# Optimization experiments

Hardware: AMD Instinct MI355X
Metric: run time of the kernel (lower is better)

## Reference

```python
import jax, jax.numpy as jnp
import numpy as np

MARGIN = 0.3
HARD_FACTOR = 0.0
EPS = 1e-6


def setup_inputs() -> dict:
    key = jax.random.key(0)
    k1, k2 = jax.random.split(key)
    inputs = jax.random.normal(k1, (4096, 256), dtype=jnp.float32)
    targets = jax.random.randint(k2, (4096,), 0, 512, dtype=jnp.int64)
    return {"inputs": inputs, "targets": targets}


def reference(inputs, targets):
    n = inputs.shape[0]
    half = n // 2
    # L2-normalize features (matches normalize(): x / (||x|| + 1e-6))
    x = inputs / (jnp.linalg.norm(inputs, axis=-1, keepdims=True) + EPS)
    # pairwise euclidean distances, clamped at 1e-6 before sqrt
    sq = jnp.sum(x * x, axis=1)                      # (n,)
    dist = sq[:, None] + sq[None, :] - 2.0 * (x @ x.T)  # (n, n)
    dist = jnp.sqrt(jnp.clip(dist, EPS))
    # same-identity mask
    mask = targets[:, None] == targets[None, :]      # (n, n) bool
    # rows in the first half mine over columns [half:n], rows in the
    # second half mine over columns [0:half] -> gather the opposite half
    first = (jnp.arange(n) < half)[:, None]          # (n, 1)
    d_o = jnp.where(first, dist[:, half:], dist[:, :half])  # (n, half)
    m_o = jnp.where(first, mask[:, half:], mask[:, :half])  # (n, half) bool
    pos_any = jnp.any(m_o, axis=1)
    neg_any = jnp.any(~m_o, axis=1)
    dist_ap = jnp.where(pos_any,
                        jnp.max(jnp.where(m_o, d_o, -jnp.inf), axis=1),
                        0.0)
    dist_an = jnp.where(neg_any,
                        jnp.min(jnp.where(m_o, jnp.inf, d_o), axis=1),
                        1.0)
    dist_ap = dist_ap * (1.0 + HARD_FACTOR)
    dist_an = dist_an * (1.0 - HARD_FACTOR)
    # MarginRankingLoss(margin)(dist_an, dist_ap, y=1) =
    #   mean(relu(-(dist_an - dist_ap) + margin))
    loss = jnp.mean(jax.nn.relu(dist_ap - dist_an + MARGIN))
    return loss
```

## Files before the change

### kernel.cpp

```cpp
#include <hip/hip_runtime.h>
#include <math.h>

#define N 4096
#define D 256
#define HALF 2048
#define MARGIN 0.3f

#define BM 64
#define NTB (HALF/BM)
#define LDA 264

typedef __attribute__((ext_vector_type(8))) short bf16x8;
typedef __attribute__((ext_vector_type(4))) float f32x4;

__device__ __forceinline__ unsigned short bf16_rne(float x) {
    unsigned int u = __float_as_uint(x);
    return (unsigned short)((u + 0x7fffu + ((u >> 16) & 1u)) >> 16);
}

__global__ __launch_bounds__(256) void k_norm(const float* __restrict__ in,
                                              unsigned short* __restrict__ xnb,
                                              float* __restrict__ sq,
                                              float* __restrict__ acc_sum,
                                              int* __restrict__ acc_cnt) {
    const int wave = threadIdx.x >> 6, lane = threadIdx.x & 63;
    const int row = blockIdx.x * 4 + wave;
    float4 v = *(const float4*)&in[(size_t)row * D + lane * 4];
    float s = v.x * v.x + v.y * v.y + v.z * v.z + v.w * v.w;
#pragma unroll
    for (int o = 1; o < 64; o <<= 1) s += __shfl_xor(s, o, 64);
    float nrm = sqrtf(s);
    float inv = 1.0f / (nrm + 1e-6f);
    ushort4 h;
    h.x = bf16_rne(v.x * inv);
    h.y = bf16_rne(v.y * inv);
    h.z = bf16_rne(v.z * inv);
    h.w = bf16_rne(v.w * inv);
    *(ushort4*)&xnb[(size_t)row * D + lane * 4] = h;
    if (lane == 0) {
        float q = nrm * inv;
        sq[row] = q * q;
    }
    if (blockIdx.x == 0 && threadIdx.x == 0) {
        *acc_sum = 0.f;
        *acc_cnt = 0;
    }
}

__global__ __launch_bounds__(256) void k_tile(const unsigned short* __restrict__ xnb,
                                              const float* __restrict__ sq,
                                              const int* __restrict__ tg,
                                              float* __restrict__ rowap,
                                              float* __restrict__ rowan,
                                              float* __restrict__ colap,
                                              float* __restrict__ colan) {
    __shared__ unsigned short As[BM * LDA];
    __shared__ unsigned short Bs[BM * LDA];
    __shared__ int sra[BM], srn[BM], sca[BM], scn[BM];

    const int bi = blockIdx.y, bj = blockIdx.x;
    const int I0 = bi * BM;
    const int J0 = bj * BM;
    const int tid = threadIdx.x;
    const int wave = tid >> 6, lane = tid & 63;
    const int wm = wave >> 1, wn = wave & 1;
    const int lrow = lane & 15, lquad = lane >> 4;

    {
        const int chunk = tid & 31;
        const int rp = tid >> 5;
        const unsigned short* Agp = xnb + (size_t)I0 * D;
        const unsigned short* Bgp = xnb + (size_t)(HALF + J0) * D;
        uint4 av[8], bv[8];
#pragma unroll
        for (int i = 0; i < 8; ++i) {
            int r = i * 8 + rp;
            av[i] = *(const uint4*)&Agp[(size_t)r * D + chunk * 8];
            bv[i] = *(const uint4*)&Bgp[(size_t)r * D + chunk * 8];
        }
#pragma unroll
        for (int i = 0; i < 8; ++i) {
            int r = i * 8 + rp;
            *(uint4*)&As[r * LDA + chunk * 8] = av[i];
            *(uint4*)&Bs[r * LDA + chunk * 8] = bv[i];
        }
    }
    __syncthreads();

    f32x4 acc[2][2];
#pragma unroll
    for (int a = 0; a < 2; ++a)
#pragma unroll
        for (int b = 0; b < 2; ++b) acc[a][b] = (f32x4){0.f, 0.f, 0.f, 0.f};

#pragma unroll
    for (int k0 = 0; k0 < D; k0 += 32) {
        bf16x8 af[2], bfr[2];
#pragma unroll
        for (int mi = 0; mi < 2; ++mi)
            af[mi] = *(const bf16x8*)&As[(wm * 32 + mi * 16 + lrow) * LDA + k0 + lquad * 8];
#pragma unroll
        for (int nj = 0; nj < 2; ++nj)
            bfr[nj] = *(const bf16x8*)&Bs[(wn * 32 + nj * 16 + lrow) * LDA + k0 + lquad * 8];
#pragma unroll
        for (int mi = 0; mi < 2; ++mi)
#pragma unroll
            for (int nj = 0; nj < 2; ++nj)
                acc[mi][nj] = __builtin_amdgcn_mfma_f32_16x16x32_bf16(
                    af[mi], bfr[nj], acc[mi][nj], 0, 0, 0);
    }

    float sqi[2][4], sqj[2];
    int tgi[2][4], tgj[2];
#pragma unroll
    for (int mi = 0; mi < 2; ++mi)
#pragma unroll
        for (int r = 0; r < 4; ++r) {
            int lr = wm * 32 + mi * 16 + lquad * 4 + r;
            sqi[mi][r] = sq[I0 + lr];
            tgi[mi][r] = tg[I0 + lr];
        }
#pragma unroll
    for (int nj = 0; nj < 2; ++nj) {
        int lc = wn * 32 + nj * 16 + lrow;
        sqj[nj] = sq[HALF + J0 + lc];
        tgj[nj] = tg[HALF + J0 + lc];
    }

    const float INF = __int_as_float(0x7f800000);
    float rap[2][4], ran[2][4], capv[2], canv[2];
#pragma unroll
    for (int mi = 0; mi < 2; ++mi)
#pragma unroll
        for (int r = 0; r < 4; ++r) { rap[mi][r] = 0.f; ran[mi][r] = INF; }
#pragma unroll
    for (int nj = 0; nj < 2; ++nj) { capv[nj] = 0.f; canv[nj] = INF; }

#pragma unroll
    for (int mi = 0; mi < 2; ++mi)
#pragma unroll
        for (int nj = 0; nj < 2; ++nj)
#pragma unroll
            for (int r = 0; r < 4; ++r) {
                float d2 = sqi[mi][r] + sqj[nj] - 2.0f * acc[mi][nj][r];
                float d = sqrtf(fmaxf(d2, 1e-6f));
                if (tgi[mi][r] == tgj[nj]) {
                    rap[mi][r] = fmaxf(rap[mi][r], d);
                    capv[nj] = fmaxf(capv[nj], d);
                } else {
                    ran[mi][r] = fminf(ran[mi][r], d);
                    canv[nj] = fminf(canv[nj], d);
                }
            }

#pragma unroll
    for (int mi = 0; mi < 2; ++mi)
#pragma unroll
        for (int r = 0; r < 4; ++r)
#pragma unroll
            for (int o = 1; o < 16; o <<= 1) {
                rap[mi][r] = fmaxf(rap[mi][r], __shfl_xor(rap[mi][r], o, 64));
                ran[mi][r] = fminf(ran[mi][r], __shfl_xor(ran[mi][r], o, 64));
            }
#pragma unroll
    for (int nj = 0; nj < 2; ++nj)
#pragma unroll
        for (int o = 16; o < 64; o <<= 1) {
            capv[nj] = fmaxf(capv[nj], __shfl_xor(capv[nj], o, 64));
            canv[nj] = fminf(canv[nj], __shfl_xor(canv[nj], o, 64));
        }

    if (tid < BM) { sra[tid] = 0; srn[tid] = 0x7f800000;
                    sca[tid] = 0; scn[tid] = 0x7f800000; }
    __syncthreads();
    if (lrow == 0) {
#pragma unroll
        for (int mi = 0; mi < 2; ++mi)
#pragma unroll
            for (int r = 0; r < 4; ++r) {
                int lr = wm * 32 + mi * 16 + lquad * 4 + r;
                atomicMax(&sra[lr], __float_as_int(rap[mi][r]));
                atomicMin(&srn[lr], __float_as_int(ran[mi][r]));
            }
    }
    if (lquad == 0) {
#pragma unroll
        for (int nj = 0; nj < 2; ++nj) {
            int lc = wn * 32 + nj * 16 + lrow;
            atomicMax(&sca[lc], __float_as_int(capv[nj]));
            atomicMin(&scn[lc], __float_as_int(canv[nj]));
        }
    }
    __syncthreads();
    if (tid < BM) {
        rowap[bj * HALF + I0 + tid] = __int_as_float(sra[tid]);
        rowan[bj * HALF + I0 + tid] = __int_as_float(srn[tid]);
        colap[bi * HALF + J0 + tid] = __int_as_float(sca[tid]);
        colan[bi * HALF + J0 + tid] = __int_as_float(scn[tid]);
    }
}

__global__ __launch_bounds__(64) void k_reduce(const float* __restrict__ rowap,
                                               const float* __restrict__ rowan,
                                               const float* __restrict__ colap,
                                               const float* __restrict__ colan,
                                               float* __restrict__ acc_sum,
                                               int* __restrict__ acc_cnt,
                                               float* __restrict__ out) {
    const int lane = threadIdx.x;
    const int gid = blockIdx.x * 64 + lane;
    const float INF = __int_as_float(0x7f800000);
    float ap = 0.f, an = INF;
    if (gid < HALF) {
#pragma unroll
        for (int b = 0; b < NTB; ++b) {
            ap = fmaxf(ap, rowap[b * HALF + gid]);
            an = fminf(an, rowan[b * HALF + gid]);
        }
    } else {
        int j = gid - HALF;
#pragma unroll
        for (int b = 0; b < NTB; ++b) {
            ap = fmaxf(ap, colap[b * HALF + j]);
            an = fminf(an, colan[b * HALF + j]);
        }
    }
    if (an == INF) an = 1.0f;
    float v = ap - an + MARGIN;
    float s = (v > 0.f) ? v : 0.f;
#pragma unroll
    for (int o = 1; o < 64; o <<= 1) s += __shfl_xor(s, o, 64);
    if (lane == 0) {
        atomicAdd(acc_sum, s);
        __threadfence();
        int old = atomicAdd(acc_cnt, 1);
        if (old == 63) {
            float tot = atomicAdd(acc_sum, 0.0f);
            out[0] = tot / (float)N;
        }
    }
}

extern "C" void kernel_launch(void* const* d_in, const int* in_sizes, int n_in,
                              void* d_out, int out_size, void* d_ws, size_t ws_size,
                              hipStream_t stream) {
    const float* in = (const float*)d_in[0];
    const int* tg = (const int*)d_in[1];
    float* out = (float*)d_out;

    unsigned short* xnb = (unsigned short*)d_ws;
    float* sq = (float*)(xnb + (size_t)N * D);
    float* rowap = sq + N;
    float* rowan = rowap + NTB * HALF;
    float* colap = rowan + NTB * HALF;
    float* colan = colap + NTB * HALF;
    float* acc_sum = colan + NTB * HALF;
    int* acc_cnt = (int*)(acc_sum + 1);

    k_norm<<<N / 4, 256, 0, stream>>>(in, xnb, sq, acc_sum, acc_cnt);
    k_tile<<<dim3(NTB, NTB), 256, 0, stream>>>(xnb, sq, tg,
                                               rowap, rowan, colap, colan);
    k_reduce<<<64, 64, 0, stream>>>(rowap, rowan, colap, colan,
                                    acc_sum, acc_cnt, out);
}
```

Baseline: 82.44 us.

## Load MFMA operands directly from global and reduce row/col extrema via global atomics

Drops the LDS staging of the A and B tiles, so each wave loads its bf16 fragments straight from global memory (relying on L1/L2 reuse) and the block no longer needs the large shared buffers or the staging barrier. Replaces the per-tile partial max/min arrays and the strided reduction in k_reduce with global integer atomicMax/atomicMin into per-row arrays, initialized in k_norm. This cuts workspace traffic and the reduction cost, but adds atomic contention (32 blocks per row) and uncoalesced, redundant global fragment loads.

```diff
diff --git a/kernel.cpp b/kernel.cpp
--- a/kernel.cpp
+++ b/kernel.cpp
@@ -8,7 +8,6 @@
 
 #define BM 64
 #define NTB (HALF/BM)
-#define LDA 264
 
 typedef __attribute__((ext_vector_type(8))) short bf16x8;
 typedef __attribute__((ext_vector_type(4))) float f32x4;
@@ -21,6 +20,8 @@
 __global__ __launch_bounds__(256) void k_norm(const float* __restrict__ in,
                                               unsigned short* __restrict__ xnb,
                                               float* __restrict__ sq,
+                                              int* __restrict__ ap,
+                                              int* __restrict__ an,
                                               float* __restrict__ acc_sum,
                                               int* __restrict__ acc_cnt) {
     const int wave = threadIdx.x >> 6, lane = threadIdx.x & 63;
@@ -40,6 +41,8 @@
     if (lane == 0) {
         float q = nrm * inv;
         sq[row] = q * q;
+        ap[row] = 0;
+        an[row] = 0x7f800000;
     }
     if (blockIdx.x == 0 && threadIdx.x == 0) {
         *acc_sum = 0.f;
@@ -50,12 +53,8 @@
 __global__ __launch_bounds__(256) void k_tile(const unsigned short* __restrict__ xnb,
                                               const float* __restrict__ sq,
                                               const int* __restrict__ tg,
-                                              float* __restrict__ rowap,
-                                              float* __restrict__ rowan,
-                                              float* __restrict__ colap,
-                                              float* __restrict__ colan) {
-    __shared__ unsigned short As[BM * LDA];
-    __shared__ unsigned short Bs[BM * LDA];
+                                              int* __restrict__ ap,
+                                              int* __restrict__ an) {
     __shared__ int sra[BM], srn[BM], sca[BM], scn[BM];
 
     const int bi = blockIdx.y, bj = blockIdx.x;
@@ -66,26 +65,10 @@
     const int wm = wave >> 1, wn = wave & 1;
     const int lrow = lane & 15, lquad = lane >> 4;
 
-    {
-        const int chunk = tid & 31;
-        const int rp = tid >> 5;
-        const unsigned short* Agp = xnb + (size_t)I0 * D;
-        const unsigned short* Bgp = xnb + (size_t)(HALF + J0) * D;
-        uint4 av[8], bv[8];
-#pragma unroll
-        for (int i = 0; i < 8; ++i) {
-            int r = i * 8 + rp;
-            av[i] = *(const uint4*)&Agp[(size_t)r * D + chunk * 8];
-            bv[i] = *(const uint4*)&Bgp[(size_t)r * D + chunk * 8];
-        }
-#pragma unroll
-        for (int i = 0; i < 8; ++i) {
-            int r = i * 8 + rp;
-            *(uint4*)&As[r * LDA + chunk * 8] = av[i];
-            *(uint4*)&Bs[r * LDA + chunk * 8] = bv[i];
-        }
-    }
-    __syncthreads();
+    const unsigned short* A0 = xnb + (size_t)(I0 + wm * 32 + lrow) * D + lquad * 8;
+    const unsigned short* A1 = A0 + (size_t)16 * D;
+    const unsigned short* B0 = xnb + (size_t)(HALF + J0 + wn * 32 + lrow) * D + lquad * 8;
+    const unsigned short* B1 = B0 + (size_t)16 * D;
 
     f32x4 acc[2][2];
 #pragma unroll
@@ -95,19 +78,14 @@
 
 #pragma unroll
     for (int k0 = 0; k0 < D; k0 += 32) {
-        bf16x8 af[2], bfr[2];
-#pragma unroll
-        for (int mi = 0; mi < 2; ++mi)
-            af[mi] = *(const bf16x8*)&As[(wm * 32 + mi * 16 + lrow) * LDA + k0 + lquad * 8];
-#pragma unroll
-        for (int nj = 0; nj < 2; ++nj)
-            bfr[nj] = *(const bf16x8*)&Bs[(wn * 32 + nj * 16 + lrow) * LDA + k0 + lquad * 8];
-#pragma unroll
-        for (int mi = 0; mi < 2; ++mi)
-#pragma unroll
-            for (int nj = 0; nj < 2; ++nj)
-                acc[mi][nj] = __builtin_amdgcn_mfma_f32_16x16x32_bf16(
-                    af[mi], bfr[nj], acc[mi][nj], 0, 0, 0);
+        bf16x8 a0 = *(const bf16x8*)(A0 + k0);
+        bf16x8 a1 = *(const bf16x8*)(A1 + k0);
+        bf16x8 b0 = *(const bf16x8*)(B0 + k0);
+        bf16x8 b1 = *(const bf16x8*)(B1 + k0);
+        acc[0][0] = __builtin_amdgcn_mfma_f32_16x16x32_bf16(a0, b0, acc[0][0], 0, 0, 0);
+        acc[0][1] = __builtin_amdgcn_mfma_f32_16x16x32_bf16(a0, b1, acc[0][1], 0, 0, 0);
+        acc[1][0] = __builtin_amdgcn_mfma_f32_16x16x32_bf16(a1, b0, acc[1][0], 0, 0, 0);
+        acc[1][1] = __builtin_amdgcn_mfma_f32_16x16x32_bf16(a1, b1, acc[1][1], 0, 0, 0);
     }
 
     float sqi[2][4], sqj[2];
@@ -193,40 +171,24 @@
     }
     __syncthreads();
     if (tid < BM) {
-        rowap[bj * HALF + I0 + tid] = __int_as_float(sra[tid]);
-        rowan[bj * HALF + I0 + tid] = __int_as_float(srn[tid]);
-        colap[bi * HALF + J0 + tid] = __int_as_float(sca[tid]);
-        colan[bi * HALF + J0 + tid] = __int_as_float(scn[tid]);
-    }
-}
-
-__global__ __launch_bounds__(64) void k_reduce(const float* __restrict__ rowap,
-                                               const float* __restrict__ rowan,
-                                               const float* __restrict__ colap,
-                                               const float* __restrict__ colan,
+        atomicMax(&ap[I0 + tid], sra[tid]);
+        atomicMin(&an[I0 + tid], srn[tid]);
+        atomicMax(&ap[HALF + J0 + tid], sca[tid]);
+        atomicMin(&an[HALF + J0 + tid], scn[tid]);
+    }
+}
+
+__global__ __launch_bounds__(64) void k_reduce(const int* __restrict__ ap,
+                                               const int* __restrict__ an,
                                                float* __restrict__ acc_sum,
                                                int* __restrict__ acc_cnt,
                                                float* __restrict__ out) {
     const int lane = threadIdx.x;
     const int gid = blockIdx.x * 64 + lane;
-    const float INF = __int_as_float(0x7f800000);
-    float ap = 0.f, an = INF;
-    if (gid < HALF) {
-#pragma unroll
-        for (int b = 0; b < NTB; ++b) {
-            ap = fmaxf(ap, rowap[b * HALF + gid]);
-            an = fminf(an, rowan[b * HALF + gid]);
-        }
-    } else {
-        int j = gid - HALF;
-#pragma unroll
-        for (int b = 0; b < NTB; ++b) {
-            ap = fmaxf(ap, colap[b * HALF + j]);
-            an = fminf(an, colan[b * HALF + j]);
-        }
-    }
-    if (an == INF) an = 1.0f;
-    float v = ap - an + MARGIN;
+    float dap = __int_as_float(ap[gid]);
+    int anb = an[gid];
+    float dan = (anb == 0x7f800000) ? 1.0f : __int_as_float(anb);
+    float v = dap - dan + MARGIN;
     float s = (v > 0.f) ? v : 0.f;
 #pragma unroll
     for (int o = 1; o < 64; o <<= 1) s += __shfl_xor(s, o, 64);
@@ -250,16 +212,12 @@
 
     unsigned short* xnb = (unsigned short*)d_ws;
     float* sq = (float*)(xnb + (size_t)N * D);
-    float* rowap = sq + N;
-    float* rowan = rowap + NTB * HALF;
-    float* colap = rowan + NTB * HALF;
-    float* colan = colap + NTB * HALF;
-    float* acc_sum = colan + NTB * HALF;
+    int* ap = (int*)(sq + N);
+    int* an = ap + N;
+    float* acc_sum = (float*)(an + N);
     int* acc_cnt = (int*)(acc_sum + 1);
 
-    k_norm<<<N / 4, 256, 0, stream>>>(in, xnb, sq, acc_sum, acc_cnt);
-    k_tile<<<dim3(NTB, NTB), 256, 0, stream>>>(xnb, sq, tg,
-                                               rowap, rowan, colap, colan);
-    k_reduce<<<64, 64, 0, stream>>>(rowap, rowan, colap, colan,
-                                    acc_sum, acc_cnt, out);
-}
+    k_norm<<<N / 4, 256, 0, stream>>>(in, xnb, sq, ap, an, acc_sum, acc_cnt);
+    k_tile<<<dim3(NTB, NTB), 256, 0, stream>>>(xnb, sq, tg, ap, an);
+    k_reduce<<<64, 64, 0, stream>>>(ap, an, acc_sum, acc_cnt, out);
+}
```

Result: faster. 80.24 us (-2.7%).
